# Kernel tuning notes

Measured on AMD Instinct MI355X. Metric: run time of the kernel, lower is better.

Reference implementation:

```python
import jax, jax.numpy as jnp
import numpy as np

H = 4                      # num_heads hard-coded in SDHGNN
NAMES = ["self", "cross", "self", "cross"]
POOL_SIZES = [2, 2, 2, 2]
MIN_NGHS = 128             # minium_nghs
EPS = 1e-3                 # InstanceNorm1d eps


def _pw(x, W, b):
    # pointwise Conv1d(kernel=1): [B, Cin, N] -> [B, Cout, N]
    return jnp.einsum('oi,bin->bon', W, x) + b[None, :, None]


def _instnorm(x):
    # InstanceNorm1d (no affine): normalize over N per (B, C)
    m = jnp.mean(x, axis=2, keepdims=True)
    v = jnp.mean((x - m) ** 2, axis=2, keepdims=True)
    return (x - m) * jax.lax.rsqrt(v + EPS)


def _attn_prop(x, src, p):
    # SharedAttentionalPropagation (sharing_attention=False):
    # MultiHeadedAttention + concat + MLP residual update.
    Wq, bq, Wk, bk, Wv, bv, Wm, bm, W1, b1, W2, b2 = p
    B, D, N = x.shape
    dh = D // H
    q = _pw(x, Wq, bq).reshape(B, dh, H, N)
    k = _pw(src, Wk, bk).reshape(B, dh, H, -1)
    v = _pw(src, Wv, bv).reshape(B, dh, H, -1)
    scores = jnp.einsum('bdhn,bdhm->bhnm', q, k) * (dh ** -0.5)
    prob = jax.nn.softmax(scores, axis=-1)                     # [B,H,N,M]
    msg = jnp.einsum('bhnm,bdhm->bdhn', prob, v).reshape(B, D, N)
    msg = _pw(msg, Wm, bm)
    y = jnp.concatenate([x, msg], axis=1)                      # [B,2D,N]
    h = jax.nn.relu(_instnorm(_pw(y, W1, b1)))
    return x + _pw(h, W2, b2), prob


def _gather(x, idx):
    # x: [B,D,N], idx: [B,K] -> [B,D,K]
    return jnp.take_along_axis(
        x, jnp.broadcast_to(idx[:, None, :], (x.shape[0], x.shape[1], idx.shape[1])), axis=2)


def _pool(prob, idx, pool_size):
    # pooling_by_prob (4-D prob branch): mean over heads, sum over queries,
    # top-k by importance, sorted indices, gather global indexes.
    K = idx.shape[1]
    p = prob.mean(axis=1).sum(axis=1)                          # [B,K]
    k = min(max(K // pool_size, MIN_NGHS), K)
    _, top = jax.lax.top_k(p, k)
    top = jnp.sort(top, axis=1)
    return jnp.take_along_axis(idx, top, axis=1)


def setup_inputs() -> dict:
    key = jax.random.key(0)
    B, D, N, L = 2, 128, 2048, 4
    ks = jax.random.split(key, 16)
    s = lambda fan: 1.0 / np.sqrt(fan)
    inp = {
        'x0': jax.random.normal(ks[0], (B, D, N), jnp.float32),
        'x1': jax.random.normal(ks[1], (B, D, N), jnp.float32),
        'Wq': jax.random.normal(ks[2], (L, D, D), jnp.float32) * s(D),
        'bq': jax.random.normal(ks[3], (L, D), jnp.float32) * 0.01,
        'Wk': jax.random.normal(ks[4], (L, D, D), jnp.float32) * s(D),
        'bk': jax.random.normal(ks[5], (L, D), jnp.float32) * 0.01,
        'Wv': jax.random.normal(ks[6], (L, D, D), jnp.float32) * s(D),
        'bv': jax.random.normal(ks[7], (L, D), jnp.float32) * 0.01,
        'Wm': jax.random.normal(ks[8], (L, D, D), jnp.float32) * s(D),
        'bm': jax.random.normal(ks[9], (L, D), jnp.float32) * 0.01,
        'W1': jax.random.normal(ks[10], (L, 2 * D, 2 * D), jnp.float32) * s(2 * D),
        'b1': jax.random.normal(ks[11], (L, 2 * D), jnp.float32) * 0.01,
        'W2': jax.random.normal(ks[12], (L, D, 2 * D), jnp.float32) * s(2 * D),
        'b2': jnp.zeros((L, D), jnp.float32),  # nn.init.constant_(mlp[-1].bias, 0)
    }
    return inp


def reference(x0, x1, Wq, bq, Wk, bk, Wv, bv, Wm, bm, W1, b1, W2, b2):
    B, D, N = x0.shape
    idx0 = jnp.broadcast_to(jnp.arange(N, dtype=jnp.int32)[None], (B, N))
    idx1 = idx0
    for l, (name, ps) in enumerate(zip(NAMES, POOL_SIZES)):
        p = (Wq[l], bq[l], Wk[l], bk[l], Wv[l], bv[l],
             Wm[l], bm[l], W1[l], b1[l], W2[l], b2[l])
        if name == 'self':
            s0, s1 = _gather(x0, idx0), _gather(x1, idx1)
        else:
            s0, s1 = _gather(x1, idx1), _gather(x0, idx0)
        x0, prob0 = _attn_prop(x0, s0, p)
        x1, prob1 = _attn_prop(x1, s1, p)
        if name == 'self':
            idx0 = _pool(prob0, idx0, ps)
            idx1 = _pool(prob1, idx1, ps)
        else:
            idx1 = _pool(prob0, idx1, ps)
            idx0 = _pool(prob1, idx0, ps)
    return jnp.stack([x0, x1], axis=0)   # [2, B, D, N]
```

## Files before the change

### kernel.cpp

```cpp
#include <hip/hip_runtime.h>
#include <cstdint>
#include <cstddef>


#define NB 2
#define ND 128
#define NH 4
#define NN 2048
#define ND2 256
#define DN (ND*NN)
#define BDN (NB*DN)
#define QK_SCALE 0.2550348623f
#define IN_EPS 1e-3f

typedef unsigned short u16;
typedef __attribute__((ext_vector_type(8))) short short8;
typedef __attribute__((ext_vector_type(4))) float f32x4;

__device__ __forceinline__ u16 f2bf(float f) {
    unsigned u = __float_as_uint(f);
    return (u16)((u + 0x7fffu + ((u >> 16) & 1u)) >> 16);
}
__device__ __forceinline__ float bf2f(u16 h) {
    return __uint_as_float(((unsigned)h) << 16);
}
__device__ __forceinline__ float fexp2(float x) {
#if __has_builtin(__builtin_amdgcn_exp2f)
    return __builtin_amdgcn_exp2f(x);
#else
    return exp2f(x);
#endif
}
__device__ __forceinline__ unsigned cvtpk_bf16(float a, float b) {
    unsigned r;
    asm("v_cvt_pk_bf16_f32 %0, %1, %2" : "=v"(r) : "v"(a), "v"(b));
    return r;
}

__global__ __launch_bounds__(256) void init_kernel(
    const float* __restrict__ x0in, const float* __restrict__ x1in,
    float* __restrict__ out, int* __restrict__ idx0, int* __restrict__ idx1)
{
    int tid = blockIdx.x * 256 + threadIdx.x;
    const float4* a = (const float4*)x0in;
    const float4* b = (const float4*)x1in;
    float4* o = (float4*)out;
    o[tid] = a[tid];
    o[BDN/4 + tid] = b[tid];
    if (tid < NB*NN) {
        int v = tid & (NN-1);
        idx0[tid] = v;
        idx1[tid] = v;
    }
}

__global__ __launch_bounds__(256) void wrepack2_kernel(
    const float* __restrict__ Wq, const float* __restrict__ Wk,
    const float* __restrict__ Wv, const float* __restrict__ Wm,
    const float* __restrict__ W1, const float* __restrict__ W2,
    const float* __restrict__ bq, const float* __restrict__ bk,
    const float* __restrict__ bv, const float* __restrict__ bm,
    const float* __restrict__ b1,
    u16* __restrict__ whi, u16* __restrict__ wlo,
    float* __restrict__ bqp, float* __restrict__ bkp, float* __restrict__ bvp,
    float* __restrict__ b1p)
{
    int e = blockIdx.x * 256 + threadIdx.x;
    if (e < 655360) {
        int l = e / 163840, r = e - l*163840;
        float v;
        if (r < 49152) {
            int m = r >> 14;
            int rr = r & 16383;
            int o = rr >> 7, c = rr & 127;
            int so = (o & 31)*4 + (o >> 5);
            const float* W = (m == 0) ? Wq : ((m == 1) ? Wk : Wv);
            v = W[l*16384 + so*128 + c];
        } else if (r < 65536) {
            int rr = r - 49152;
            int o = rr >> 7, c = rr & 127;
            int sc = (c & 31)*4 + (c >> 5);
            v = Wm[l*16384 + o*128 + sc];
        } else if (r < 131072) {
            int rr = r - 65536;
            int c = rr & 255;
            if (c < 128) {
                v = W1[l*65536 + rr];
            } else {
                int o = rr >> 8, cc = c - 128;
                int sc = (cc & 31)*4 + (cc >> 5);
                const float* w1row = &W1[l*65536 + o*256 + 128];
                const float* wmcol = &Wm[l*16384 + sc];
                float acc = 0.f;
                #pragma unroll 4
                for (int k = 0; k < 128; ++k)
                    acc = fmaf(w1row[k], wmcol[k*128], acc);
                v = acc;
            }
        }
        else                   v = W2[l*32768 + r - 131072];
        u16 hb = f2bf(v);
        whi[e] = hb;
        wlo[e] = f2bf(v - bf2f(hb));
    } else if (e < 656896) {
        int eb = e - 655360;
        int l = eb / 384, rr = eb % 384;
        int which = rr >> 7, o = rr & 127;
        int so = (o & 31)*4 + (o >> 5);
        float v = (which == 0 ? bq : (which == 1 ? bk : bv))[l*128 + so];
        (which == 0 ? bqp : (which == 1 ? bkp : bvp))[l*128 + o] = v;
    } else if (e < 657920) {
        int idx = e - 656896;
        int l = idx >> 8, o = idx & 255;
        const float* w1row = &W1[l*65536 + o*256 + 128];
        const float* bmv = &bm[l*128];
        float acc = b1[l*256 + o];
        #pragma unroll 4
        for (int k = 0; k < 128; ++k)
            acc = fmaf(w1row[k], bmv[k], acc);
        b1p[l*256 + o] = acc;
    }
}

__global__ __launch_bounds__(256) void repack_xh_kernel(
    const float* __restrict__ in, u16* __restrict__ ohi, u16* __restrict__ olo)
{
    __shared__ float tile[32][68];
    int z = blockIdx.y >> 2, cg = blockIdx.y & 3;
    int n0 = blockIdx.x * 64;
    int t = threadIdx.x;
    {
        int i = t >> 3, nc = (t & 7) * 8;
        const float* src = &in[((size_t)z*128 + cg*32 + i)*NN + n0 + nc];
        float4 a = *(const float4*)src;
        float4 b = *(const float4*)(src + 4);
        tile[i][nc+0]=a.x; tile[i][nc+1]=a.y; tile[i][nc+2]=a.z; tile[i][nc+3]=a.w;
        tile[i][nc+4]=b.x; tile[i][nc+5]=b.y; tile[i][nc+6]=b.z; tile[i][nc+7]=b.w;
    }
    __syncthreads();
    int n = t >> 2, c8 = (t & 3) * 8;
    short8 hi, lo;
    #pragma unroll
    for (int j = 0; j < 8; ++j) {
        float v = tile[c8 + j][n];
        u16 h = f2bf(v);
        hi[j] = (short)h;
        lo[j] = (short)f2bf(v - bf2f(h));
    }
    size_t ob = ((size_t)z*NN + n0 + n)*128 + cg*32 + c8;
    *(short8*)&ohi[ob] = hi;
    *(short8*)&olo[ob] = lo;
}

__device__ __forceinline__ void gcore(
    u16* As0, u16* As1, u16* Bs0, u16* Bs1,
    const u16* __restrict__ Whi, const u16* __restrict__ Wlo, int o0, int Cin,
    const u16* __restrict__ B1hi, const u16* __restrict__ B1lo, int s1,
    const u16* __restrict__ B2hi, const u16* __restrict__ B2lo, int s2, int split,
    size_t brow, int n0, const int* __restrict__ idxp, int t, f32x4 acc[2][2])
{
    const int lane = t & 63, w = t >> 6;
    const int l15 = lane & 15, quad = lane >> 4;
    const int wr = (w & 1)*32, wc = (w >> 1)*32;
    const int ao = t >> 2, ak = (t & 3)*8;
    int grow = n0 + ao;
    if (idxp) grow = idxp[grow];

    short8 rA0, rA1, rB0, rB1;
    {
        size_t wa = (size_t)(o0 + ao)*Cin + ak;
        rA0 = *(const short8*)&Whi[wa];
        rA1 = *(const short8*)&Wlo[wa];
        int c = ak;
        const u16 *ph, *pl; size_t off;
        if (c < split) { ph = B1hi; pl = B1lo; off = (brow + grow)*s1 + c; }
        else { ph = B2hi; pl = B2lo; off = (brow + grow)*s2 + (c - split); }
        rB0 = *(const short8*)&ph[off];
        rB1 = *(const short8*)&pl[off];
    }
    for (int kc = 0; kc < Cin; kc += 32) {
        __syncthreads();
        *(short8*)&As0[ao*40 + ak] = rA0;
        *(short8*)&As1[ao*40 + ak] = rA1;
        *(short8*)&Bs0[ao*40 + ak] = rB0;
        *(short8*)&Bs1[ao*40 + ak] = rB1;
        if (kc + 32 < Cin) {
            size_t wa = (size_t)(o0 + ao)*Cin + kc + 32 + ak;
            rA0 = *(const short8*)&Whi[wa];
            rA1 = *(const short8*)&Wlo[wa];
            int c = kc + 32 + ak;
            const u16 *ph, *pl; size_t off;
            if (c < split) { ph = B1hi; pl = B1lo; off = (brow + grow)*s1 + c; }
            else { ph = B2hi; pl = B2lo; off = (brow + grow)*s2 + (c - split); }
            rB0 = *(const short8*)&ph[off];
            rB1 = *(const short8*)&pl[off];
        }
        __syncthreads();
        short8 Ah[2], Al[2], Bh[2], Bl[2];
        #pragma unroll
        for (int a = 0; a < 2; ++a) {
            Ah[a] = *(const short8*)&As0[(wr + a*16 + l15)*40 + quad*8];
            Al[a] = *(const short8*)&As1[(wr + a*16 + l15)*40 + quad*8];
        }
        #pragma unroll
        for (int c = 0; c < 2; ++c) {
            Bh[c] = *(const short8*)&Bs0[(wc + c*16 + l15)*40 + quad*8];
            Bl[c] = *(const short8*)&Bs1[(wc + c*16 + l15)*40 + quad*8];
        }
        #pragma unroll
        for (int a = 0; a < 2; ++a)
            #pragma unroll
            for (int c = 0; c < 2; ++c) {
                acc[a][c] = __builtin_amdgcn_mfma_f32_16x16x32_bf16(Ah[a], Bl[c], acc[a][c], 0,0,0);
                acc[a][c] = __builtin_amdgcn_mfma_f32_16x16x32_bf16(Al[a], Bh[c], acc[a][c], 0,0,0);
                acc[a][c] = __builtin_amdgcn_mfma_f32_16x16x32_bf16(Ah[a], Bh[c], acc[a][c], 0,0,0);
            }
    }
    __syncthreads();
}

__global__ __launch_bounds__(256) void qkv_kernel(
    const u16* __restrict__ Whi, const u16* __restrict__ Wlo,
    const float* __restrict__ bqp, const float* __restrict__ bkp,
    const float* __restrict__ bvp,
    const u16* __restrict__ xphi, const u16* __restrict__ xplo,
    const int* __restrict__ idx0, const int* __restrict__ idx1,
    int cross, int M,
    u16* __restrict__ qthi, u16* __restrict__ qtlo,
    u16* __restrict__ kthi, u16* __restrict__ ktlo,
    u16* __restrict__ vthi, float* __restrict__ p,
    float* __restrict__ gsum, float* __restrict__ gsq)
{
    __shared__ u16 gsm[10240];
    u16* As0 = gsm;  u16* As1 = gsm + 2560;
    u16* Bs0 = gsm + 5120; u16* Bs1 = gsm + 7680;
    float* tb = (float*)gsm;

    const int z = blockIdx.z;
    const int bx = blockIdx.x;
    const int t = threadIdx.x;
    const int lane = t & 63, w = t >> 6;
    const int l15 = lane & 15, quad = lane >> 4;
    const int wr = (w & 1)*32, wc = (w >> 1)*32;

    int role, o0, n0, nCols;
    const u16 *Wbh, *Wbl;
    const float* bias;
    if (bx < 64) {
        role = 0; o0 = (bx & 1)*64; n0 = (bx >> 1)*64; nCols = NN;
        Wbh = Whi; Wbl = Wlo; bias = bqp;
        if (t < 32) p[(size_t)z*NN + bx*32 + t] = 0.f;
        if (bx == 0) { gsum[z*256 + t] = 0.f; gsq[z*256 + t] = 0.f; }
    } else {
        int e = bx - 64;
        int kt = M >> 6;
        int ct = e % kt, rt = e / kt;
        n0 = ct*64; nCols = M;
        if (rt < 2) { role = 1; o0 = rt*64; Wbh = Whi+16384; Wbl = Wlo+16384; bias = bkp; }
        else        { role = 2; o0 = (rt-2)*64; Wbh = Whi+32768; Wbl = Wlo+32768; bias = bvp; }
    }
    size_t brow = (size_t)z * NN;
    const int* idxp = nullptr;
    if (role != 0) {
        int ss = cross ? 1 - (z >> 1) : (z >> 1);
        brow = (size_t)(ss*2 + (z & 1)) * NN;
        idxp = (ss ? idx1 : idx0) + (z & 1)*NN;
    }

    f32x4 acc[2][2];
    #pragma unroll
    for (int a = 0; a < 2; ++a)
        #pragma unroll
        for (int c = 0; c < 2; ++c) acc[a][c] = (f32x4){0.f,0.f,0.f,0.f};

    gcore(As0, As1, Bs0, Bs1, Wbh, Wbl, o0, 128,
          xphi, xplo, 128, xphi, xplo, 128, 128, brow, n0, idxp, t, acc);

    if (role == 2) {
        #pragma unroll
        for (int a = 0; a < 2; ++a)
            #pragma unroll
            for (int c = 0; c < 2; ++c)
                #pragma unroll
                for (int r = 0; r < 4; ++r) {
                    int row = o0 + wr + a*16 + quad*4 + r;
                    int m = n0 + wc + c*16 + l15;
                    float v = acc[a][c][r] + bias[row];
                    vthi[((size_t)(z*4 + (row>>5))*32 + (row&31))*(size_t)M + m] = f2bf(v);
                }
    } else {
        float scale = role ? 1.f : QK_SCALE;
        #pragma unroll
        for (int a = 0; a < 2; ++a)
            #pragma unroll
            for (int c = 0; c < 2; ++c)
                #pragma unroll
                for (int r = 0; r < 4; ++r) {
                    int rl = wr + a*16 + quad*4 + r;
                    tb[rl*66 + wc + c*16 + l15] = acc[a][c][r] + bias[o0 + rl];
                }
        __syncthreads();
        u16* ohi = role ? kthi : qthi;
        u16* olo = role ? ktlo : qtlo;
        int n = t >> 2, rb = (t & 3)*16;
        #pragma unroll
        for (int g = 0; g < 2; ++g) {
            short8 hi, lo;
            #pragma unroll
            for (int j = 0; j < 8; ++j) {
                float v = tb[(rb + g*8 + j)*66 + n] * scale;
                u16 hb = f2bf(v);
                hi[j] = (short)hb;
                lo[j] = (short)f2bf(v - bf2f(hb));
            }
            int rowg = o0 + rb + g*8;
            size_t ob = ((size_t)(z*4 + (rowg >> 5))*nCols + n0 + n)*32 + (rowg & 31);
            *(short8*)&ohi[ob] = hi;
            *(short8*)&olo[ob] = lo;
        }
    }
}

__global__ __launch_bounds__(512, 4) void attn4_kernel(
    const u16* __restrict__ qthi, const u16* __restrict__ qtlo,
    const u16* __restrict__ kthi, const u16* __restrict__ ktlo,
    const u16* __restrict__ vthi, int M,
    u16* __restrict__ msghi, u16* __restrict__ msglo, float* __restrict__ p)
{
    __shared__ float pcol[2048];
    __shared__ float obuf[96*66];
    __shared__ float redm[4][64], redl[4][64];
    __shared__ float rowM[64], rowIV[64];

    const int t = threadIdx.x;
    const int lane = t & 63, wave = t >> 6;
    const int l15 = lane & 15, quad = lane >> 4;
    const int qp = wave & 1, mh = wave >> 1;
    const int h = blockIdx.y, z = blockIdx.z;
    const int zh = z*4 + h;
    const int n0 = blockIdx.x * 64;

    for (int i = t; i < M; i += 512) pcol[i] = 0.f;

    short8 qBh[2], qBl[2];
    #pragma unroll
    for (int qt = 0; qt < 2; ++qt) {
        size_t qb = ((size_t)zh*NN + n0 + qp*32 + qt*16 + l15)*32 + quad*8;
        qBh[qt] = *(const short8*)&qthi[qb];
        qBl[qt] = *(const short8*)&qtlo[qb];
    }

    const int nch = M >> 7;
    const size_t kb0 = ((size_t)zh*M + mh*32 + l15)*32 + quad*8;
    const u16* kbh = kthi + kb0;
    const u16* kbl = ktlo + kb0;
    const u16* vb = vthi + ((size_t)zh*32 + l15)*M + mh*32 + quad*8;

    float rm[2] = {-1e30f, -1e30f}, rl[2] = {0.f, 0.f};

    for (int ch = 0; ch < nch; ++ch) {
        const int co = ch*128*32;
        #pragma unroll
        for (int mt = 0; mt < 2; ++mt) {
            short8 kh = *(const short8*)&kbh[co + mt*512];
            short8 kl = *(const short8*)&kbl[co + mt*512];
            __builtin_amdgcn_s_setprio(1);
            f32x4 av[2];
            #pragma unroll
            for (int qt = 0; qt < 2; ++qt) {
                f32x4 a = {0.f,0.f,0.f,0.f};
                a = __builtin_amdgcn_mfma_f32_16x16x32_bf16(kh, qBl[qt], a, 0,0,0);
                a = __builtin_amdgcn_mfma_f32_16x16x32_bf16(kl, qBh[qt], a, 0,0,0);
                a = __builtin_amdgcn_mfma_f32_16x16x32_bf16(kh, qBh[qt], a, 0,0,0);
                av[qt] = a;
            }
            __builtin_amdgcn_s_setprio(0);
            #pragma unroll
            for (int qt = 0; qt < 2; ++qt) {
                f32x4 a = av[qt];
                float bm = fmaxf(fmaxf(a[0],a[1]), fmaxf(a[2],a[3]));
                float bs = fexp2(a[0]-bm)+fexp2(a[1]-bm)+fexp2(a[2]-bm)+fexp2(a[3]-bm);
                if (bm > rm[qt]) { rl[qt] = rl[qt]*fexp2(rm[qt]-bm) + bs; rm[qt] = bm; }
                else rl[qt] += bs*fexp2(bm - rm[qt]);
            }
        }
    }

    #pragma unroll
    for (int qt = 0; qt < 2; ++qt) {
        #pragma unroll
        for (int off = 16; off <= 32; off <<= 1) {
            float om = __shfl_xor(rm[qt], off);
            float ol = __shfl_xor(rl[qt], off);
            float nm = fmaxf(rm[qt], om);
            rl[qt] = rl[qt]*fexp2(rm[qt]-nm) + ol*fexp2(om-nm);
            rm[qt] = nm;
        }
        if (quad == 0) {
            redm[mh][qp*32 + qt*16 + l15] = rm[qt];
            redl[mh][qp*32 + qt*16 + l15] = rl[qt];
        }
    }
    __syncthreads();
    if (t < 64) {
        float m = redm[0][t], l = redl[0][t];
        #pragma unroll
        for (int w2 = 1; w2 < 4; ++w2) {
            float om = redm[w2][t];
            float nm = fmaxf(m, om);
            l = l*fexp2(m - nm) + redl[w2][t]*fexp2(om - nm);
            m = nm;
        }
        rowM[t] = m;
        rowIV[t] = 1.f / l;
    }
    __syncthreads();
    float myRM[2], myRIV[2];
    #pragma unroll
    for (int qt = 0; qt < 2; ++qt) {
        myRM[qt]  = rowM[qp*32 + qt*16 + l15];
        myRIV[qt] = rowIV[qp*32 + qt*16 + l15];
    }

    f32x4 oa[2][2];
    #pragma unroll
    for (int qt = 0; qt < 2; ++qt)
        #pragma unroll
        for (int dt = 0; dt < 2; ++dt) oa[qt][dt] = (f32x4){0.f,0.f,0.f,0.f};

    const int aA = (l15 + 32*(quad & 1))*4;
    const int aB = aA + 64;
    const bool mtsel = (quad >= 2);

    for (int ch = 0; ch < nch; ++ch) {
        const int m0 = ch << 7;
        const int co = ch*128*32;

        float pr[2][2][4];
        #pragma unroll
        for (int mt = 0; mt < 2; ++mt) {
            short8 kh = *(const short8*)&kbh[co + mt*512];
            short8 kl = *(const short8*)&kbl[co + mt*512];
            __builtin_amdgcn_s_setprio(1);
            f32x4 av[2];
            #pragma unroll
            for (int qt = 0; qt < 2; ++qt) {
                f32x4 a = {0.f,0.f,0.f,0.f};
                a = __builtin_amdgcn_mfma_f32_16x16x32_bf16(kh, qBl[qt], a, 0,0,0);
                a = __builtin_amdgcn_mfma_f32_16x16x32_bf16(kl, qBh[qt], a, 0,0,0);
                a = __builtin_amdgcn_mfma_f32_16x16x32_bf16(kh, qBh[qt], a, 0,0,0);
                av[qt] = a;
            }
            __builtin_amdgcn_s_setprio(0);
            #pragma unroll
            for (int qt = 0; qt < 2; ++qt)
                #pragma unroll
                for (int r = 0; r < 4; ++r)
                    pr[qt][mt][r] = fexp2(av[qt][r] - myRM[qt]);
        }

        #pragma unroll
        for (int mt = 0; mt < 2; ++mt)
            #pragma unroll
            for (int r = 0; r < 4; ++r) {
                float ps = pr[0][mt][r]*myRIV[0] + pr[1][mt][r]*myRIV[1];
                ps += __shfl_xor(ps, 1);
                ps += __shfl_xor(ps, 2);
                ps += __shfl_xor(ps, 4);
                ps += __shfl_xor(ps, 8);
                if (l15 == 0)
                    atomicAdd(&pcol[m0 + mh*32 + mt*16 + quad*4 + r], ps);
            }

        short8 vA[2];
        #pragma unroll
        for (int dt = 0; dt < 2; ++dt)
            vA[dt] = *(const short8*)&vb[(size_t)dt*16*M + m0];

        #pragma unroll
        for (int qt = 0; qt < 2; ++qt) {
            unsigned pk00 = cvtpk_bf16(pr[qt][0][0], pr[qt][0][1]);
            unsigned pk01 = cvtpk_bf16(pr[qt][0][2], pr[qt][0][3]);
            unsigned pk10 = cvtpk_bf16(pr[qt][1][0], pr[qt][1][1]);
            unsigned pk11 = cvtpk_bf16(pr[qt][1][2], pr[qt][1][3]);
            unsigned a0 = (unsigned)__builtin_amdgcn_ds_bpermute(aA, (int)pk00);
            unsigned a1 = (unsigned)__builtin_amdgcn_ds_bpermute(aA, (int)pk01);
            unsigned a2 = (unsigned)__builtin_amdgcn_ds_bpermute(aA, (int)pk10);
            unsigned a3 = (unsigned)__builtin_amdgcn_ds_bpermute(aA, (int)pk11);
            unsigned b0 = (unsigned)__builtin_amdgcn_ds_bpermute(aB, (int)pk00);
            unsigned b1 = (unsigned)__builtin_amdgcn_ds_bpermute(aB, (int)pk01);
            unsigned b2 = (unsigned)__builtin_amdgcn_ds_bpermute(aB, (int)pk10);
            unsigned b3 = (unsigned)__builtin_amdgcn_ds_bpermute(aB, (int)pk11);
            union { unsigned u[4]; short8 s; } fb;
            fb.u[0] = mtsel ? a2 : a0;
            fb.u[1] = mtsel ? a3 : a1;
            fb.u[2] = mtsel ? b2 : b0;
            fb.u[3] = mtsel ? b3 : b1;
            __builtin_amdgcn_s_setprio(1);
            #pragma unroll
            for (int dt = 0; dt < 2; ++dt)
                oa[qt][dt] = __builtin_amdgcn_mfma_f32_16x16x32_bf16(vA[dt], fb.s, oa[qt][dt], 0,0,0);
            __builtin_amdgcn_s_setprio(0);
        }
    }

    if (mh > 0) {
        #pragma unroll
        for (int qt = 0; qt < 2; ++qt)
            #pragma unroll
            for (int dt = 0; dt < 2; ++dt)
                #pragma unroll
                for (int r = 0; r < 4; ++r) {
                    int q = qp*32 + qt*16 + l15;
                    int d = dt*16 + quad*4 + r;
                    obuf[((mh-1)*32 + d)*66 + q] = oa[qt][dt][r];
                }
    }
    __syncthreads();
    if (mh == 0) {
        #pragma unroll
        for (int qt = 0; qt < 2; ++qt)
            #pragma unroll
            for (int dt = 0; dt < 2; ++dt)
                #pragma unroll
                for (int r = 0; r < 4; ++r) {
                    int q = qp*32 + qt*16 + l15;
                    int d = dt*16 + quad*4 + r;
                    float v = oa[qt][dt][r];
                    #pragma unroll
                    for (int w2 = 0; w2 < 3; ++w2)
                        v += obuf[(w2*32 + d)*66 + q];
                    obuf[d*66 + q] = v * myRIV[qt];
                }
    }
    __syncthreads();
    {
        int tt = t & 255;
        int n = tt >> 2, i8 = (tt & 3)*8;
        short8 o8;
        if (t < 256) {
            #pragma unroll
            for (int j = 0; j < 8; ++j) o8[j] = (short)f2bf(obuf[(i8+j)*66 + n]);
            *(short8*)&msghi[((size_t)z*NN + n0 + n)*128 + h*32 + i8] = o8;
        } else {
            #pragma unroll
            for (int j = 0; j < 8; ++j) {
                float v = obuf[(i8+j)*66 + n];
                u16 hb = f2bf(v);
                o8[j] = (short)f2bf(v - bf2f(hb));
            }
            *(short8*)&msglo[((size_t)z*NN + n0 + n)*128 + h*32 + i8] = o8;
        }
    }
    for (int i = t; i < M; i += 512)
        atomicAdd(&p[(size_t)z*NN + i], pcol[i]*0.25f);
}

__global__ __launch_bounds__(256) void w1_kernel(
    const u16* __restrict__ W1h, const u16* __restrict__ W1l,
    const float* __restrict__ b1,
    const u16* __restrict__ xphi, const u16* __restrict__ xplo,
    const u16* __restrict__ m2hi, const u16* __restrict__ m2lo,
    float* __restrict__ zf, float* __restrict__ gsum, float* __restrict__ gsq)
{
    __shared__ u16 gsm[10240];
    u16* As0 = gsm;  u16* As1 = gsm + 2560;
    u16* Bs0 = gsm + 5120; u16* Bs1 = gsm + 7680;

    const int z = blockIdx.z, o0 = blockIdx.y*64, n0 = blockIdx.x*64;
    const int t = threadIdx.x;
    const int lane = t & 63, w = t >> 6;
    const int l15 = lane & 15, quad = lane >> 4;
    const int wr = (w & 1)*32, wc = (w >> 1)*32;

    f32x4 acc[2][2];
    #pragma unroll
    for (int a = 0; a < 2; ++a)
        #pragma unroll
        for (int c = 0; c < 2; ++c) acc[a][c] = (f32x4){0.f,0.f,0.f,0.f};
    gcore(As0, As1, Bs0, Bs1, W1h, W1l, o0, 256,
          xphi, xplo, 128, m2hi, m2lo, 128, 128,
          (size_t)z*NN, n0, nullptr, t, acc);

    float ssum[2][4], ssq[2][4];
    #pragma unroll
    for (int a = 0; a < 2; ++a)
        #pragma unroll
        for (int r = 0; r < 4; ++r) { ssum[a][r] = 0.f; ssq[a][r] = 0.f; }
    #pragma unroll
    for (int a = 0; a < 2; ++a)
        #pragma unroll
        for (int c = 0; c < 2; ++c)
            #pragma unroll
            for (int r = 0; r < 4; ++r) {
                int row = o0 + wr + a*16 + quad*4 + r;
                int n = n0 + wc + c*16 + l15;
                float v = acc[a][c][r] + b1[row];
                zf[((size_t)z*256 + row)*NN + n] = v;
                ssum[a][r] += v;
                ssq[a][r] = fmaf(v, v, ssq[a][r]);
            }
    #pragma unroll
    for (int a = 0; a < 2; ++a)
        #pragma unroll
        for (int r = 0; r < 4; ++r) {
            float s = ssum[a][r], q2 = ssq[a][r];
            #pragma unroll
            for (int o = 1; o < 16; o <<= 1) {
                s  += __shfl_xor(s, o);
                q2 += __shfl_xor(q2, o);
            }
            if (l15 == 0) {
                int row = o0 + wr + a*16 + quad*4 + r;
                atomicAdd(&gsum[z*256 + row], s);
                atomicAdd(&gsq[z*256 + row], q2);
            }
        }
}

__global__ __launch_bounds__(256) void hrepack_kernel(
    const float* __restrict__ zf, const float* __restrict__ gsum,
    const float* __restrict__ gsq, u16* __restrict__ hhi, u16* __restrict__ hlo)
{
    __shared__ float tile[32][68];
    int z = blockIdx.y >> 3, cg = blockIdx.y & 7;
    int n0 = blockIdx.x * 64;
    int t = threadIdx.x;
    {
        int i = t >> 3, nc = (t & 7) * 8;
        int c = cg*32 + i;
        float mean = gsum[z*256 + c] * (1.f/NN);
        float var = gsq[z*256 + c] * (1.f/NN) - mean*mean;
        float iv = rsqrtf(var + IN_EPS);
        const float* src = &zf[((size_t)z*256 + c)*NN + n0 + nc];
        float4 a = *(const float4*)src;
        float4 b = *(const float4*)(src + 4);
        float vv[8] = {a.x,a.y,a.z,a.w,b.x,b.y,b.z,b.w};
        #pragma unroll
        for (int j = 0; j < 8; ++j) {
            float v = (vv[j] - mean) * iv;
            tile[i][nc + j] = v > 0.f ? v : 0.f;
        }
    }
    __syncthreads();
    int n = t >> 2, c8 = (t & 3) * 8;
    short8 hi, lo;
    #pragma unroll
    for (int j = 0; j < 8; ++j) {
        float v = tile[c8 + j][n];
        u16 hb = f2bf(v);
        hi[j] = (short)hb;
        lo[j] = (short)f2bf(v - bf2f(hb));
    }
    size_t ob = ((size_t)z*NN + n0 + n)*256 + cg*32 + c8;
    *(short8*)&hhi[ob] = hi;
    *(short8*)&hlo[ob] = lo;
}

__global__ __launch_bounds__(256) void w2_kernel(
    const u16* __restrict__ W2h, const u16* __restrict__ W2l,
    const float* __restrict__ b2,
    const u16* __restrict__ hhi, const u16* __restrict__ hlo,
    float* __restrict__ out, u16* __restrict__ xphi, u16* __restrict__ xplo,
    int writeplanes)
{
    __shared__ u16 gsm[10240];
    u16* As0 = gsm;  u16* As1 = gsm + 2560;
    u16* Bs0 = gsm + 5120; u16* Bs1 = gsm + 7680;
    float* tb = (float*)gsm;

    const int z = blockIdx.z, o0 = blockIdx.y*64, n0 = blockIdx.x*64;
    const int t = threadIdx.x;
    const int lane = t & 63, w = t >> 6;
    const int l15 = lane & 15, quad = lane >> 4;
    const int wr = (w & 1)*32, wc = (w >> 1)*32;

    f32x4 acc[2][2];
    #pragma unroll
    for (int a = 0; a < 2; ++a)
        #pragma unroll
        for (int c = 0; c < 2; ++c) acc[a][c] = (f32x4){0.f,0.f,0.f,0.f};
    gcore(As0, As1, Bs0, Bs1, W2h, W2l, o0, 256,
          hhi, hlo, 256, hhi, hlo, 256, 256,
          (size_t)z*NN, n0, nullptr, t, acc);

    #pragma unroll
    for (int a = 0; a < 2; ++a)
        #pragma unroll
        for (int c = 0; c < 2; ++c)
            #pragma unroll
            for (int r = 0; r < 4; ++r) {
                int rl = wr + a*16 + quad*4 + r;
                int rowg = o0 + rl;
                int n = n0 + wc + c*16 + l15;
                size_t oi = ((size_t)z*128 + rowg)*NN + n;
                float v = acc[a][c][r] + b2[rowg] + out[oi];
                out[oi] = v;
                tb[rl*66 + wc + c*16 + l15] = v;
            }
    __syncthreads();
    if (writeplanes) {
        int n = t >> 2, rb = (t & 3)*16;
        #pragma unroll
        for (int g = 0; g < 2; ++g) {
            short8 hi, lo;
            #pragma unroll
            for (int j = 0; j < 8; ++j) {
                float v = tb[(rb + g*8 + j)*66 + n];
                u16 hb = f2bf(v);
                hi[j] = (short)hb;
                lo[j] = (short)f2bf(v - bf2f(hb));
            }
            size_t ob = ((size_t)z*NN + n0 + n)*128 + o0 + rb + g*8;
            *(short8*)&xphi[ob] = hi;
            *(short8*)&xplo[ob] = lo;
        }
    }
}

__global__ __launch_bounds__(256) void rank_kernel(
    const float* __restrict__ p, int* __restrict__ rank, int M)
{
    int zz = blockIdx.y;
    __shared__ float pv[2048];
    for (int i = threadIdx.x; i < M; i += 256) pv[i] = p[(size_t)zz*NN + i];
    __syncthreads();
    int i = blockIdx.x * 256 + threadIdx.x;
    if (i < M) {
        float pi = pv[i];
        int r = 0;
        for (int j = 0; j < M; ++j) {
            float pj = pv[j];
            r += (pj > pi) ? 1 : ((pj == pi && j < i) ? 1 : 0);
        }
        rank[zz*NN + i] = r;
    }
}

__global__ __launch_bounds__(256) void select_kernel(
    const int* __restrict__ rank, int* __restrict__ idx0, int* __restrict__ idx1,
    int M, int k, int cross)
{
    int z = blockIdx.x;
    int st = z >> 1, b = z & 1;
    int ts = cross ? 1 - st : st;
    int* idx = (ts ? idx1 : idx0) + b * NN;
    const int* rk = rank + z * NN;
    __shared__ int sel[2048], idv[2048], sa[2048], sb[2048];
    int t = threadIdx.x;
    for (int i = t; i < M; i += 256) {
        int s = rk[i] < k ? 1 : 0;
        sel[i] = s;
        sa[i] = s;
        idv[i] = idx[i];
    }
    __syncthreads();
    int* src = sa; int* dst = sb;
    for (int off = 1; off < M; off <<= 1) {
        for (int i = t; i < M; i += 256)
            dst[i] = src[i] + (i >= off ? src[i - off] : 0);
        __syncthreads();
        int* tmp = src; src = dst; dst = tmp;
    }
    for (int i = t; i < M; i += 256)
        if (sel[i]) idx[src[i] - 1] = idv[i];
}

extern "C" void kernel_launch(void* const* d_in, const int* in_sizes, int n_in,
                              void* d_out, int out_size, void* d_ws, size_t ws_size,
                              hipStream_t stream)
{
    const float* x0in = (const float*)d_in[0];
    const float* x1in = (const float*)d_in[1];
    const float* Wq = (const float*)d_in[2];
    const float* bq = (const float*)d_in[3];
    const float* Wk = (const float*)d_in[4];
    const float* bk = (const float*)d_in[5];
    const float* Wv = (const float*)d_in[6];
    const float* bv = (const float*)d_in[7];
    const float* Wm = (const float*)d_in[8];
    const float* bm = (const float*)d_in[9];
    const float* W1 = (const float*)d_in[10];
    const float* b1 = (const float*)d_in[11];
    const float* W2 = (const float*)d_in[12];
    const float* b2 = (const float*)d_in[13];

    float* out = (float*)d_out;
    float* ws  = (float*)d_ws;

    const size_t U = 1048576;
    u16* ub   = (u16*)ws;
    u16* xphi = ub;            u16* xplo = ub + U;
    u16* qthi = ub + 2*U;      u16* qtlo = ub + 3*U;
    u16* kthi = ub + 4*U;      u16* ktlo = ub + 5*U;
    u16* vthi = ub + 6*U;
    u16* msghi = ub + 7*U;     u16* msglo = ub + 8*U;
    u16* m2hi = ub + 9*U;      u16* m2lo = ub + 10*U;
    u16* hhi  = ub + 11*U;     u16* hlo = ub + 13*U;
    u16* whi  = ub + 15*U;     u16* wlo = whi + 655360;
    float* zf = (float*)(ub + 2*U);
    float* ft = (float*)(wlo + 655360);
    float* bqp = ft;           float* bkp = ft + 512;      float* bvp = ft + 1024;
    float* gsum = ft + 1536;   float* gsq = ft + 2560;
    float* p = ft + 3584;
    int* idx0 = (int*)(p + 4*NN);
    int* idx1 = idx0 + NB*NN;
    int* rankb = idx1 + NB*NN;
    float* b1p = (float*)(rankb + 4*NN);

    init_kernel<<<BDN/4/256, 256, 0, stream>>>(x0in, x1in, out, idx0, idx1);
    wrepack2_kernel<<<2570, 256, 0, stream>>>(Wq, Wk, Wv, Wm, W1, W2, bq, bk, bv,
                                              bm, b1, whi, wlo, bqp, bkp, bvp, b1p);
    repack_xh_kernel<<<dim3(32, 16), 256, 0, stream>>>(out, xphi, xplo);

    const int Ms[4] = {2048, 1024, 512, 256};
    for (int l = 0; l < 4; ++l) {
        int M = Ms[l];
        int k_new = (M/2 < 128) ? 128 : M/2;
        int cross = l & 1;
        size_t lw = (size_t)l * 163840;
        const u16* Wlh = whi + lw;  const u16* Wll = wlo + lw;

        qkv_kernel<<<dim3(64 + 4*(M/64), 1, 4), 256, 0, stream>>>(
            Wlh, Wll, bqp + l*128, bkp + l*128, bvp + l*128,
            xphi, xplo, idx0, idx1, cross, M,
            qthi, qtlo, kthi, ktlo, vthi, p, gsum, gsq);

        attn4_kernel<<<dim3(32, NH, 4), 512, 0, stream>>>(
            qthi, qtlo, kthi, ktlo, vthi, M, msghi, msglo, p);

        w1_kernel<<<dim3(32, 4, 4), 256, 0, stream>>>(
            Wlh + 65536, Wll + 65536, b1p + l*256,
            xphi, xplo, msghi, msglo, zf, gsum, gsq);

        hrepack_kernel<<<dim3(32, 32), 256, 0, stream>>>(zf, gsum, gsq, hhi, hlo);

        w2_kernel<<<dim3(32, 2, 4), 256, 0, stream>>>(
            Wlh + 131072, Wll + 131072, b2 + l*128,
            hhi, hlo, out, xphi, xplo, (l < 3) ? 1 : 0);

        rank_kernel<<<dim3((M+255)/256, 4), 256, 0, stream>>>(p, rankb, M);
        select_kernel<<<4, 256, 0, stream>>>(rankb, idx0, idx1, M, k_new, cross);
    }
}
```

Before: 534.6 us.

## Fuse instance-norm repack into W2 GEMM load and merge rank/select kernels

```diff
diff --git a/kernel.cpp b/kernel.cpp
--- a/kernel.cpp
+++ b/kernel.cpp
@@ -219,6 +219,88 @@
     __syncthreads();
 }
 
+__device__ __forceinline__ void gcore_w2(
+    u16* As0, u16* As1, u16* Bs0, u16* Bs1,
+    const u16* __restrict__ Whi, const u16* __restrict__ Wlo, int o0,
+    const float* __restrict__ zft, const float* __restrict__ meanL,
+    const float* __restrict__ ivL,
+    size_t brow, int n0, int t, f32x4 acc[2][2])
+{
+    const int Cin = 256;
+    const int lane = t & 63, w = t >> 6;
+    const int l15 = lane & 15, quad = lane >> 4;
+    const int wr = (w & 1)*32, wc = (w >> 1)*32;
+    const int ao = t >> 2, ak = (t & 3)*8;
+    const float* brows = &zft[(brow + n0 + ao)*256];
+
+    short8 rA0, rA1, rBh, rBl;
+    {
+        size_t wa = (size_t)(o0 + ao)*Cin + ak;
+        rA0 = *(const short8*)&Whi[wa];
+        rA1 = *(const short8*)&Wlo[wa];
+        float4 f0 = *(const float4*)&brows[ak];
+        float4 f1 = *(const float4*)&brows[ak + 4];
+        float f[8] = {f0.x,f0.y,f0.z,f0.w,f1.x,f1.y,f1.z,f1.w};
+        #pragma unroll
+        for (int j = 0; j < 8; ++j) {
+            float v = (f[j] - meanL[ak + j]) * ivL[ak + j];
+            v = v > 0.f ? v : 0.f;
+            u16 hb = f2bf(v);
+            rBh[j] = (short)hb;
+            rBl[j] = (short)f2bf(v - bf2f(hb));
+        }
+    }
+    for (int kc = 0; kc < Cin; kc += 32) {
+        __syncthreads();
+        *(short8*)&As0[ao*40 + ak] = rA0;
+        *(short8*)&As1[ao*40 + ak] = rA1;
+        *(short8*)&Bs0[ao*40 + ak] = rBh;
+        *(short8*)&Bs1[ao*40 + ak] = rBl;
+        float4 f0n, f1n;
+        const bool more = (kc + 32 < Cin);
+        if (more) {
+            size_t wa = (size_t)(o0 + ao)*Cin + kc + 32 + ak;
+            rA0 = *(const short8*)&Whi[wa];
+            rA1 = *(const short8*)&Wlo[wa];
+            f0n = *(const float4*)&brows[kc + 32 + ak];
+            f1n = *(const float4*)&brows[kc + 32 + ak + 4];
+        }
+        __syncthreads();
+        short8 Ah[2], Al[2], Bh[2], Bl[2];
+        #pragma unroll
+        for (int a = 0; a < 2; ++a) {
+            Ah[a] = *(const short8*)&As0[(wr + a*16 + l15)*40 + quad*8];
+            Al[a] = *(const short8*)&As1[(wr + a*16 + l15)*40 + quad*8];
+        }
+        #pragma unroll
+        for (int c = 0; c < 2; ++c) {
+            Bh[c] = *(const short8*)&Bs0[(wc + c*16 + l15)*40 + quad*8];
+            Bl[c] = *(const short8*)&Bs1[(wc + c*16 + l15)*40 + quad*8];
+        }
+        #pragma unroll
+        for (int a = 0; a < 2; ++a)
+            #pragma unroll
+            for (int c = 0; c < 2; ++c) {
+                acc[a][c] = __builtin_amdgcn_mfma_f32_16x16x32_bf16(Ah[a], Bl[c], acc[a][c], 0,0,0);
+                acc[a][c] = __builtin_amdgcn_mfma_f32_16x16x32_bf16(Al[a], Bh[c], acc[a][c], 0,0,0);
+                acc[a][c] = __builtin_amdgcn_mfma_f32_16x16x32_bf16(Ah[a], Bh[c], acc[a][c], 0,0,0);
+            }
+        if (more) {
+            float f[8] = {f0n.x,f0n.y,f0n.z,f0n.w,f1n.x,f1n.y,f1n.z,f1n.w};
+            #pragma unroll
+            for (int j = 0; j < 8; ++j) {
+                int cc = kc + 32 + ak + j;
+                float v = (f[j] - meanL[cc]) * ivL[cc];
+                v = v > 0.f ? v : 0.f;
+                u16 hb = f2bf(v);
+                rBh[j] = (short)hb;
+                rBl[j] = (short)f2bf(v - bf2f(hb));
+            }
+        }
+    }
+    __syncthreads();
+}
+
 __global__ __launch_bounds__(256) void qkv_kernel(
     const u16* __restrict__ Whi, const u16* __restrict__ Wlo,
     const float* __restrict__ bqp, const float* __restrict__ bkp,
@@ -561,11 +643,12 @@
     const float* __restrict__ b1,
     const u16* __restrict__ xphi, const u16* __restrict__ xplo,
     const u16* __restrict__ m2hi, const u16* __restrict__ m2lo,
-    float* __restrict__ zf, float* __restrict__ gsum, float* __restrict__ gsq)
+    float* __restrict__ zft, float* __restrict__ gsum, float* __restrict__ gsq)
 {
     __shared__ u16 gsm[10240];
     u16* As0 = gsm;  u16* As1 = gsm + 2560;
     u16* Bs0 = gsm + 5120; u16* Bs1 = gsm + 7680;
+    float* tb = (float*)gsm;
 
     const int z = blockIdx.z, o0 = blockIdx.y*64, n0 = blockIdx.x*64;
     const int t = threadIdx.x;
@@ -593,10 +676,10 @@
         for (int c = 0; c < 2; ++c)
             #pragma unroll
             for (int r = 0; r < 4; ++r) {
-                int row = o0 + wr + a*16 + quad*4 + r;
-                int n = n0 + wc + c*16 + l15;
-                float v = acc[a][c][r] + b1[row];
-                zf[((size_t)z*256 + row)*NN + n] = v;
+                int rl = wr + a*16 + quad*4 + r;
+                int cl = wc + c*16 + l15;
+                float v = acc[a][c][r] + b1[o0 + rl];
+                tb[rl*66 + cl] = v;
                 ssum[a][r] += v;
                 ssq[a][r] = fmaf(v, v, ssq[a][r]);
             }
@@ -616,55 +699,35 @@
                 atomicAdd(&gsq[z*256 + row], q2);
             }
         }
-}
-
-__global__ __launch_bounds__(256) void hrepack_kernel(
-    const float* __restrict__ zf, const float* __restrict__ gsum,
-    const float* __restrict__ gsq, u16* __restrict__ hhi, u16* __restrict__ hlo)
-{
-    __shared__ float tile[32][68];
-    int z = blockIdx.y >> 3, cg = blockIdx.y & 7;
-    int n0 = blockIdx.x * 64;
-    int t = threadIdx.x;
-    {
-        int i = t >> 3, nc = (t & 7) * 8;
-        int c = cg*32 + i;
-        float mean = gsum[z*256 + c] * (1.f/NN);
-        float var = gsq[z*256 + c] * (1.f/NN) - mean*mean;
-        float iv = rsqrtf(var + IN_EPS);
-        const float* src = &zf[((size_t)z*256 + c)*NN + n0 + nc];
-        float4 a = *(const float4*)src;
-        float4 b = *(const float4*)(src + 4);
-        float vv[8] = {a.x,a.y,a.z,a.w,b.x,b.y,b.z,b.w};
-        #pragma unroll
-        for (int j = 0; j < 8; ++j) {
-            float v = (vv[j] - mean) * iv;
-            tile[i][nc + j] = v > 0.f ? v : 0.f;
-        }
-    }
-    __syncthreads();
-    int n = t >> 2, c8 = (t & 3) * 8;
-    short8 hi, lo;
-    #pragma unroll
-    for (int j = 0; j < 8; ++j) {
-        float v = tile[c8 + j][n];
-        u16 hb = f2bf(v);
-        hi[j] = (short)hb;
-        lo[j] = (short)f2bf(v - bf2f(hb));
-    }
-    size_t ob = ((size_t)z*NN + n0 + n)*256 + cg*32 + c8;
-    *(short8*)&hhi[ob] = hi;
-    *(short8*)&hlo[ob] = lo;
+    __syncthreads();
+    int n = t >> 2, rb = (t & 3)*16;
+    #pragma unroll
+    for (int g = 0; g < 2; ++g) {
+        float4 v0, v1;
+        v0.x = tb[(rb + g*8 + 0)*66 + n];
+        v0.y = tb[(rb + g*8 + 1)*66 + n];
+        v0.z = tb[(rb + g*8 + 2)*66 + n];
+        v0.w = tb[(rb + g*8 + 3)*66 + n];
+        v1.x = tb[(rb + g*8 + 4)*66 + n];
+        v1.y = tb[(rb + g*8 + 5)*66 + n];
+        v1.z = tb[(rb + g*8 + 6)*66 + n];
+        v1.w = tb[(rb + g*8 + 7)*66 + n];
+        float* dst = &zft[((size_t)z*NN + n0 + n)*256 + o0 + rb + g*8];
+        *(float4*)dst = v0;
+        *(float4*)(dst + 4) = v1;
+    }
 }
 
 __global__ __launch_bounds__(256) void w2_kernel(
     const u16* __restrict__ W2h, const u16* __restrict__ W2l,
     const float* __restrict__ b2,
-    const u16* __restrict__ hhi, const u16* __restrict__ hlo,
+    const float* __restrict__ zft, const float* __restrict__ gsum,
+    const float* __restrict__ gsq,
     float* __restrict__ out, u16* __restrict__ xphi, u16* __restrict__ xplo,
     int writeplanes)
 {
     __shared__ u16 gsm[10240];
+    __shared__ float meanL[256], ivL[256];
     u16* As0 = gsm;  u16* As1 = gsm + 2560;
     u16* Bs0 = gsm + 5120; u16* Bs1 = gsm + 7680;
     float* tb = (float*)gsm;
@@ -675,14 +738,21 @@
     const int l15 = lane & 15, quad = lane >> 4;
     const int wr = (w & 1)*32, wc = (w >> 1)*32;
 
+    {
+        float mean = gsum[z*256 + t] * (1.f/NN);
+        float var  = gsq[z*256 + t] * (1.f/NN) - mean*mean;
+        meanL[t] = mean;
+        ivL[t] = rsqrtf(var + IN_EPS);
+    }
+    __syncthreads();
+
     f32x4 acc[2][2];
     #pragma unroll
     for (int a = 0; a < 2; ++a)
         #pragma unroll
         for (int c = 0; c < 2; ++c) acc[a][c] = (f32x4){0.f,0.f,0.f,0.f};
-    gcore(As0, As1, Bs0, Bs1, W2h, W2l, o0, 256,
-          hhi, hlo, 256, hhi, hlo, 256, 256,
-          (size_t)z*NN, n0, nullptr, t, acc);
+    gcore_w2(As0, As1, Bs0, Bs1, W2h, W2l, o0,
+             zft, meanL, ivL, (size_t)z*NN, n0, t, acc);
 
     #pragma unroll
     for (int a = 0; a < 2; ++a)
@@ -718,38 +788,27 @@
     }
 }
 
-__global__ __launch_bounds__(256) void rank_kernel(
-    const float* __restrict__ p, int* __restrict__ rank, int M)
-{
-    int zz = blockIdx.y;
+__global__ __launch_bounds__(1024) void rankselect_kernel(
+    const float* __restrict__ p, int* __restrict__ idx0, int* __restrict__ idx1,
+    int M, int k, int cross)
+{
+    int z = blockIdx.x;
+    int st = z >> 1, b = z & 1;
+    int ts = cross ? 1 - st : st;
+    int* idx = (ts ? idx1 : idx0) + b * NN;
     __shared__ float pv[2048];
-    for (int i = threadIdx.x; i < M; i += 256) pv[i] = p[(size_t)zz*NN + i];
-    __syncthreads();
-    int i = blockIdx.x * 256 + threadIdx.x;
-    if (i < M) {
+    __shared__ int sel[2048], idv[2048], sa[2048], sb[2048];
+    int t = threadIdx.x;
+    for (int i = t; i < M; i += 1024) pv[i] = p[(size_t)z*NN + i];
+    __syncthreads();
+    for (int i = t; i < M; i += 1024) {
         float pi = pv[i];
         int r = 0;
         for (int j = 0; j < M; ++j) {
             float pj = pv[j];
             r += (pj > pi) ? 1 : ((pj == pi && j < i) ? 1 : 0);
         }
-        rank[zz*NN + i] = r;
-    }
-}
-
-__global__ __launch_bounds__(256) void select_kernel(
-    const int* __restrict__ rank, int* __restrict__ idx0, int* __restrict__ idx1,
-    int M, int k, int cross)
-{
-    int z = blockIdx.x;
-    int st = z >> 1, b = z & 1;
-    int ts = cross ? 1 - st : st;
-    int* idx = (ts ? idx1 : idx0) + b * NN;
-    const int* rk = rank + z * NN;
-    __shared__ int sel[2048], idv[2048], sa[2048], sb[2048];
-    int t = threadIdx.x;
-    for (int i = t; i < M; i += 256) {
-        int s = rk[i] < k ? 1 : 0;
+        int s = (r < k) ? 1 : 0;
         sel[i] = s;
         sa[i] = s;
         idv[i] = idx[i];
@@ -757,12 +816,12 @@
     __syncthreads();
     int* src = sa; int* dst = sb;
     for (int off = 1; off < M; off <<= 1) {
-        for (int i = t; i < M; i += 256)
+        for (int i = t; i < M; i += 1024)
             dst[i] = src[i] + (i >= off ? src[i - off] : 0);
         __syncthreads();
         int* tmp = src; src = dst; dst = tmp;
     }
-    for (int i = t; i < M; i += 256)
+    for (int i = t; i < M; i += 1024)
         if (sel[i]) idx[src[i] - 1] = idv[i];
 }
 
@@ -795,10 +854,8 @@
     u16* kthi = ub + 4*U;      u16* ktlo = ub + 5*U;
     u16* vthi = ub + 6*U;
     u16* msghi = ub + 7*U;     u16* msglo = ub + 8*U;
-    u16* m2hi = ub + 9*U;      u16* m2lo = ub + 10*U;
-    u16* hhi  = ub + 11*U;     u16* hlo = ub + 13*U;
     u16* whi  = ub + 15*U;     u16* wlo = whi + 655360;
-    float* zf = (float*)(ub + 2*U);
+    float* zft = (float*)(ub + 2*U);
     float* ft = (float*)(wlo + 655360);
     float* bqp = ft;           float* bkp = ft + 512;      float* bvp = ft + 1024;
     float* gsum = ft + 1536;   float* gsq = ft + 2560;
@@ -831,15 +888,12 @@
 
         w1_kernel<<<dim3(32, 4, 4), 256, 0, stream>>>(
             Wlh + 65536, Wll + 65536, b1p + l*256,
-            xphi, xplo, msghi, msglo, zf, gsum, gsq);
-
-        hrepack_kernel<<<dim3(32, 32), 256, 0, stream>>>(zf, gsum, gsq, hhi, hlo);
+            xphi, xplo, msghi, msglo, zft, gsum, gsq);
 
         w2_kernel<<<dim3(32, 2, 4), 256, 0, stream>>>(
             Wlh + 131072, Wll + 131072, b2 + l*128,
-            hhi, hlo, out, xphi, xplo, (l < 3) ? 1 : 0);
-
-        rank_kernel<<<dim3((M+255)/256, 4), 256, 0, stream>>>(p, rankb, M);
-        select_kernel<<<4, 256, 0, stream>>>(rankb, idx0, idx1, M, k_new, cross);
-    }
-}
+            zft, gsum, gsq, out, xphi, xplo, (l < 3) ? 1 : 0);
+
+        rankselect_kernel<<<4, 1024, 0, stream>>>(p, idx0, idx1, M, k_new, cross);
+    }
+}
```

Result: slower. 649.6 us (+21.5%).
